# Performance work log

Measured on AMD Instinct MI355X. Metric: run time of the kernel, lower is better.

Reference implementation:

```python
import jax, jax.numpy as jnp
import numpy as np

KS = 2        # kernel_size
DIL = 1       # dilation
FILTERS = 512
Z_DIM = 128
B, C, T = 8, 512, 4096
TZ = T + 2 * (KS - 1)


def _conv1d(x, w, b):
    # x: (B, L, Cin), w: (ks, Cin, Cout) -> VALID conv, channels-last (keras Conv1D)
    y = jax.lax.conv_general_dilated(x, w, window_strides=(1,), padding='VALID',
                                     dimension_numbers=('NWC', 'WIO', 'NWC'))
    return y + b


def _adaptor(z, w1, b1, w2, b2):
    return _conv1d(jax.nn.relu(_conv1d(z, w1, b1)), w2, b2)


def setup_inputs() -> dict:
    key = jax.random.key(0)
    ks = jax.random.split(key, 10)
    lim = np.sqrt(6.0 / FILTERS)
    u = lambda k, shp: jax.random.uniform(k, shp, jnp.float32, -lim, lim)
    return {
        'x': jax.random.normal(ks[0], (B, C, T), jnp.float32),
        'z': jax.random.normal(ks[1], (B, TZ, Z_DIM), jnp.float32),
        'ww1': u(ks[2], (KS, Z_DIM, FILTERS)), 'wb1': jnp.zeros((FILTERS,), jnp.float32),
        'ww2': u(ks[3], (KS, FILTERS, FILTERS)), 'wb2': jnp.zeros((FILTERS,), jnp.float32),
        'bw1': u(ks[4], (KS, Z_DIM, FILTERS)), 'bb1': jnp.zeros((FILTERS,), jnp.float32),
        'bw2': u(ks[5], (KS, FILTERS, FILTERS)), 'bb2': jnp.zeros((FILTERS,), jnp.float32),
    }


def reference(x, z, ww1, wb1, ww2, wb2, bw1, bb1, bw2, bb2):
    m = x.shape[1]
    t = x.shape[2]
    pad = DIL * (KS - 1)
    xp = jnp.pad(x, ((0, 0), (0, 0), (0, pad)))
    end = t + pad
    # im2col-style unfold: (B, C*KS, T)
    xu = jnp.concatenate([xp[:, :, pad - i * DIL: end - i * DIL] for i in range(KS)], axis=1)
    weights = _adaptor(z, ww1, wb1, ww2, wb2)   # (B, T, F)
    bias = _adaptor(z, bw1, bb1, bw2, bb2)      # (B, T, F)
    y = jnp.matmul(xu, weights)                 # (B, C*KS, F)
    return y[:, :m, :] + bias[:, :m, :]
```

## Files before the change

kernel.cpp:

```cpp
#include <hip/hip_runtime.h>

typedef short short8 __attribute__((ext_vector_type(8)));
typedef float float4v __attribute__((ext_vector_type(4)));
typedef __attribute__((address_space(1))) const unsigned int gu32;
typedef __attribute__((address_space(3))) unsigned int lu32;

__device__ __forceinline__ unsigned short f2bf(float f) {
  unsigned int u = __builtin_bit_cast(unsigned int, f);
  u += 0x7FFFu + ((u >> 16) & 1u);
  return (unsigned short)(u >> 16);
}
__device__ __forceinline__ float bf2f(unsigned short s) {
  return __builtin_bit_cast(float, (unsigned int)s << 16);
}

__global__ __launch_bounds__(256) void prep_fused(
    const float* __restrict__ x,
    const float* __restrict__ z,
    const float* __restrict__ ww1, const float* __restrict__ ww2,
    const float* __restrict__ bw1, const float* __restrict__ bw2,
    unsigned short* __restrict__ xs, unsigned short* __restrict__ xz,
    float* __restrict__ rs,
    unsigned short* __restrict__ w1T, unsigned short* __restrict__ w2T,
    unsigned short* __restrict__ b1T, unsigned short* __restrict__ b2T,
    unsigned short* __restrict__ zb)
{
  if (blockIdx.x < 4096) {
    __shared__ float red[4];
    long long r = blockIdx.x;
    const float* xr = x + r * 4096;
    int t0 = threadIdx.x * 16;
    float v[17];
    const float4* xr4 = (const float4*)(xr + t0);
#pragma unroll
    for (int q = 0; q < 4; ++q) {
      float4 f = xr4[q];
      v[q * 4] = f.x; v[q * 4 + 1] = f.y; v[q * 4 + 2] = f.z; v[q * 4 + 3] = f.w;
    }
    v[16] = (t0 + 16 < 4096) ? xr[t0 + 16] : 0.f;
    unsigned int spk[8], zpk[8];
    float sum = 0.f;
#pragma unroll
    for (int q = 0; q < 8; ++q) {
      unsigned short s0 = f2bf(v[2 * q + 1]);
      unsigned short s1 = f2bf(v[2 * q + 2]);
      sum += bf2f(s0);
      sum += bf2f(s1);
      spk[q] = (unsigned int)s0 | ((unsigned int)s1 << 16);
      unsigned short z0 = (t0 == 0 && q == 0) ? (unsigned short)0 : f2bf(v[2 * q]);
      unsigned short z1 = f2bf(v[2 * q + 1]);
      zpk[q] = (unsigned int)z0 | ((unsigned int)z1 << 16);
    }
    *(uint4*)(xs + r * 4096 + t0)     = *(uint4*)(spk);
    *(uint4*)(xs + r * 4096 + t0 + 8) = *(uint4*)(spk + 4);
    *(uint4*)(xz + r * 4096 + t0)     = *(uint4*)(zpk);
    *(uint4*)(xz + r * 4096 + t0 + 8) = *(uint4*)(zpk + 4);
#pragma unroll
    for (int off = 32; off > 0; off >>= 1) sum += __shfl_down(sum, off);
    if ((threadIdx.x & 63) == 0) red[threadIdx.x >> 6] = sum;
    __syncthreads();
    if (threadIdx.x == 0) rs[r] = red[0] + red[1] + red[2] + red[3];
  } else {
    int i = (blockIdx.x - 4096) * 256 + threadIdx.x;
    if (i < 131072) {
      int n = i & 511, k = i >> 9;
      w1T[n * 256 + k] = f2bf(ww1[i]);
    } else if (i < 655360) {
      int j = i - 131072; int n = j & 511, k = j >> 9;
      w2T[n * 1024 + k] = f2bf(ww2[j]);
    } else if (i < 786432) {
      int j = i - 655360; int n = j & 511, k = j >> 9;
      b1T[n * 256 + k] = f2bf(bw1[j]);
    } else if (i < 1310720) {
      int j = i - 786432; int n = j & 511, k = j >> 9;
      b2T[n * 1024 + k] = f2bf(bw2[j]);
    } else {
      int j = i - 1310720;
      zb[j] = f2bf(z[j]);
    }
  }
}

template<int BM, int BN, bool RELU, bool OBF16, bool TRANS, bool SPLITK, int NH>
__global__ __launch_bounds__(256)
void gemm_bt(const unsigned short* __restrict__ A,
             const unsigned short* __restrict__ A2,
             const unsigned short* __restrict__ Bt,
             const float* __restrict__ biasv,
             void* __restrict__ outp,
             void* __restrict__ outp2,
             int M, int Kchunk, int RPB, int EXTRA, int BSCALE,
             int nHalf, int bRowMask,
             long long bStrideB, long long outBatchStride, int outLd)
{
  constexpr int WM = BM / 2, WN = BN / 2;
  constexpr int NI = WM / 16, NJ = WN / 16;
  constexpr int AI = BM / 64;
  constexpr int BI = BN / 64;
  constexpr int SA1 = BM * 32, SB1 = BN * 32;
  constexpr int STAGE = NH * (SA1 + SB1);
  constexpr int SMEMN = TRANS ? ((128 * 136 > STAGE) ? 128 * 136 : STAGE) : STAGE;
  __shared__ unsigned short smem[SMEMN];
  unsigned short* sB0 = smem + NH * SA1;

  const int tid  = threadIdx.x;
  const int lane = tid & 63;
  const int wave = tid >> 6;
  const int wm = wave >> 1, wn = wave & 1;
  const int lr = lane & 15, quad = lane >> 4;

  const int r0 = blockIdx.x * BM;
  const int n0 = blockIdx.y * BN;
  const int bb = r0 / RPB;
  const int Ktot = SPLITK ? Kchunk * gridDim.z : Kchunk;
  const int kOff = SPLITK ? blockIdx.z * Kchunk : 0;
  const long long bOffB = (long long)bb * bStrideB;
  const unsigned short* Ae = (nHalf && n0 >= nHalf) ? A2 : A;

  const int srow = lane >> 2;
  const int sg = (lane & 3) ^ (srow & 3);
  const unsigned short* gA[AI]; unsigned short* ldsA[AI];
#pragma unroll
  for (int c = 0; c < AI; ++c) {
    int instr = c * 4 + wave;
    int row = instr * 16 + srow;
    int r = r0 + row; if (r > M - 1) r = M - 1;
    gA[c] = Ae + ((long long)r + (long long)(r / RPB) * EXTRA) * BSCALE + kOff + sg * 8;
    ldsA[c] = smem + instr * 512;
  }
  const unsigned short* gB[BI]; unsigned short* ldsB[BI];
#pragma unroll
  for (int c = 0; c < BI; ++c) {
    int instr = c * 4 + wave;
    int row = instr * 16 + srow;
    gB[c] = Bt + (long long)((n0 + row) & bRowMask) * Ktot + bOffB + kOff + sg * 8;
    ldsB[c] = sB0 + instr * 512;
  }

  int aoff[NI], boff[NJ];
#pragma unroll
  for (int i = 0; i < NI; ++i) {
    int rr = wm * WM + i * 16 + lr;
    aoff[i] = rr * 32 + ((quad ^ (rr & 3)) * 8);
  }
#pragma unroll
  for (int j = 0; j < NJ; ++j) {
    int rr = wn * WN + j * 16 + lr;
    boff[j] = rr * 32 + ((quad ^ (rr & 3)) * 8);
  }

  float4v acc[NI][NJ];
  const float4v z4 = {0.f, 0.f, 0.f, 0.f};
#pragma unroll
  for (int i = 0; i < NI; ++i)
#pragma unroll
    for (int j = 0; j < NJ; ++j) acc[i][j] = z4;

  for (int k0 = 0; k0 < Kchunk; k0 += 32 * NH) {
#pragma unroll
    for (int h = 0; h < NH; ++h) {
#pragma unroll
      for (int c = 0; c < AI; ++c)
        __builtin_amdgcn_global_load_lds((gu32*)(gA[c] + k0 + h * 32),
                                         (lu32*)(ldsA[c] + h * SA1), 16, 0, 0);
#pragma unroll
      for (int c = 0; c < BI; ++c)
        __builtin_amdgcn_global_load_lds((gu32*)(gB[c] + k0 + h * 32),
                                         (lu32*)(ldsB[c] + h * SB1), 16, 0, 0);
    }
    __syncthreads();
#pragma unroll
    for (int h = 0; h < NH; ++h) {
      short8 af[NI], bfr[NJ];
#pragma unroll
      for (int i = 0; i < NI; ++i) af[i] = *(const short8*)(smem + h * SA1 + aoff[i]);
#pragma unroll
      for (int j = 0; j < NJ; ++j) bfr[j] = *(const short8*)(sB0 + h * SB1 + boff[j]);
#pragma unroll
      for (int i = 0; i < NI; ++i)
#pragma unroll
        for (int j = 0; j < NJ; ++j)
          acc[i][j] = __builtin_amdgcn_mfma_f32_16x16x32_bf16(af[i], bfr[j], acc[i][j], 0, 0, 0);
    }
    __syncthreads();
  }

  if (TRANS) {
    unsigned short* Ts = smem;
#pragma unroll
    for (int j = 0; j < NJ; ++j) {
      int fr = wn * WN + j * 16 + lr;
      float bv = biasv[n0 + fr];
#pragma unroll
      for (int i = 0; i < NI; ++i) {
        int tr = wm * WM + i * 16 + quad * 4;
        unsigned long long pk = 0;
#pragma unroll
        for (int g = 0; g < 4; ++g) {
          float vv = acc[i][j][g] + bv;
          if (RELU) vv = fmaxf(vv, 0.f);
          pk |= (unsigned long long)f2bf(vv) << (16 * g);
        }
        *(unsigned long long*)(Ts + fr * 136 + tr) = pk;
      }
    }
    __syncthreads();
    int fr = tid >> 1, sgg = tid & 1;
    int t0l = r0 - bb * RPB;
    unsigned short* dst = (unsigned short*)outp + (long long)bb * outBatchStride
                        + (long long)(n0 + fr) * outLd + t0l + sgg * 64;
    const unsigned short* srcp = Ts + fr * 136 + sgg * 64;
#pragma unroll
    for (int u = 0; u < 8; ++u)
      *(uint4*)(dst + u * 8) = *(const uint4*)(srcp + u * 8);
  } else {
    void* op = (SPLITK && blockIdx.z) ? outp2 : outp;
#pragma unroll
    for (int j = 0; j < NJ; ++j) {
      int n_g = n0 + wn * WN + j * 16 + lr;
      float bv = biasv ? biasv[n_g] : 0.f;
#pragma unroll
      for (int i = 0; i < NI; ++i) {
        int r_base = r0 + wm * WM + i * 16 + quad * 4;
#pragma unroll
        for (int g = 0; g < 4; ++g) {
          int r_g = r_base + g;
          if (r_g >= M) continue;
          float v = acc[i][j][g] + bv;
          if (RELU) v = fmaxf(v, 0.f);
          long long oidx = (long long)r_g * outLd + n_g;
          if (OBF16) ((unsigned short*)op)[oidx] = f2bf(v);
          else       ((float*)op)[oidx] = v;
        }
      }
    }
  }
}

__global__ __launch_bounds__(256) void final_gemm3(
    const unsigned short* __restrict__ p0,
    const unsigned short* __restrict__ p1,
    const unsigned short* __restrict__ h1b,
    const unsigned short* __restrict__ w2T,
    const unsigned short* __restrict__ b2T,
    const float* __restrict__ rs,
    const float* __restrict__ wb2,
    const float* __restrict__ bb2,
    float* __restrict__ out)
{
  constexpr int SA1 = 64 * 32, SB1 = 64 * 32;
  __shared__ unsigned short smem[4 * SA1 + 4 * SB1];
  const int tid = threadIdx.x;
  const int lane = tid & 63, wave = tid >> 6;
  const int wm = wave >> 1, wn = wave & 1;
  const int lr = lane & 15, quad = lane >> 4;
  const int r0 = blockIdx.x * 64, n0 = blockIdx.y * 64;

  const int srow = lane >> 2;
  const int sg = (lane & 3) ^ (srow & 3);
  const int row = wave * 16 + srow;
  const int rA = r0 + row;
  const int rB = n0 + row;
  const unsigned short* aP[3] = {
    p0 + (long long)rA * 1024 + sg * 8,
    p1 + (long long)rA * 1024 + sg * 8,
    h1b + ((long long)rA + (rA >> 9)) * 512 + sg * 8 };
  const unsigned short* bP[3] = {
    w2T + (long long)rB * 1024 + sg * 8,
    w2T + (long long)rB * 1024 + sg * 8,
    b2T + (long long)rB * 1024 + sg * 8 };
  unsigned short* ldsA = smem + wave * 512;
  unsigned short* ldsB = smem + 4 * SA1 + wave * 512;

  int aoff[2], boff[2];
#pragma unroll
  for (int i = 0; i < 2; ++i) {
    int rr = wm * 32 + i * 16 + lr;
    aoff[i] = rr * 32 + ((quad ^ (rr & 3)) * 8);
    int nn = wn * 32 + i * 16 + lr;
    boff[i] = 4 * SA1 + nn * 32 + ((quad ^ (nn & 3)) * 8);
  }

  float4v acc[2][2];
  const float4v z4 = {0.f, 0.f, 0.f, 0.f};
  acc[0][0] = z4; acc[0][1] = z4; acc[1][0] = z4; acc[1][1] = z4;

  for (int k0 = 0; k0 < 3072; k0 += 128) {
    int seg = k0 >> 10;
    int kk = k0 & 1023;
#pragma unroll
    for (int h = 0; h < 4; ++h) {
      __builtin_amdgcn_global_load_lds((gu32*)(aP[seg] + kk + h * 32),
                                       (lu32*)(ldsA + h * SA1), 16, 0, 0);
      __builtin_amdgcn_global_load_lds((gu32*)(bP[seg] + kk + h * 32),
                                       (lu32*)(ldsB + h * SB1), 16, 0, 0);
    }
    __syncthreads();
#pragma unroll
    for (int h = 0; h < 4; ++h) {
      short8 af[2], bfr[2];
      af[0] = *(const short8*)(smem + h * SA1 + aoff[0]);
      af[1] = *(const short8*)(smem + h * SA1 + aoff[1]);
      bfr[0] = *(const short8*)(smem + h * SB1 + boff[0]);
      bfr[1] = *(const short8*)(smem + h * SB1 + boff[1]);
#pragma unroll
      for (int i = 0; i < 2; ++i)
#pragma unroll
        for (int j = 0; j < 2; ++j)
          acc[i][j] = __builtin_amdgcn_mfma_f32_16x16x32_bf16(af[i], bfr[j], acc[i][j], 0, 0, 0);
    }
    __syncthreads();
  }

#pragma unroll
  for (int j = 0; j < 2; ++j) {
    int n_g = n0 + wn * 32 + j * 16 + lr;
    float w2b = wb2[n_g], bbv = bb2[n_g];
#pragma unroll
    for (int i = 0; i < 2; ++i) {
      int rb = r0 + wm * 32 + i * 16 + quad * 4;
#pragma unroll
      for (int g = 0; g < 4; ++g) {
        int r_g = rb + g;
        out[(long long)r_g * 512 + n_g] = acc[i][j][g] + rs[r_g] * w2b + bbv;
      }
    }
  }
}

extern "C" void kernel_launch(void* const* d_in, const int* in_sizes, int n_in,
                              void* d_out, int out_size, void* d_ws, size_t ws_size,
                              hipStream_t stream) {
  const float* x   = (const float*)d_in[0];
  const float* z   = (const float*)d_in[1];
  const float* ww1 = (const float*)d_in[2];
  const float* wb1 = (const float*)d_in[3];
  const float* ww2 = (const float*)d_in[4];
  const float* wb2 = (const float*)d_in[5];
  const float* bw1 = (const float*)d_in[6];
  const float* bb1 = (const float*)d_in[7];
  const float* bw2 = (const float*)d_in[8];
  const float* bb2 = (const float*)d_in[9];

  char* ws = (char*)d_ws;
  unsigned short* xs  = (unsigned short*)ws; ws += 16777216ll * 2;
  unsigned short* xz  = (unsigned short*)ws; ws += 16777216ll * 2;
  unsigned short* zb  = (unsigned short*)ws; ws += 4196352ll  * 2;
  unsigned short* h1T = (unsigned short*)ws; ws += 16777216ll * 2;
  unsigned short* h1b = (unsigned short*)ws; ws += 2101248ll  * 2;
  unsigned short* w2T = (unsigned short*)ws; ws += 524288ll * 2;
  unsigned short* b2T = (unsigned short*)ws; ws += 524288ll * 2;
  float* rs = (float*)ws;                    ws += 4096ll * 4;
  char* tail = ws;
  unsigned short* w1T = (unsigned short*)tail;
  unsigned short* b1T = (unsigned short*)tail + 131072;
  unsigned short* p0  = zb;
  unsigned short* p1  = (unsigned short*)tail;

  prep_fused<<<4096 + 21512, 256, 0, stream>>>(
      x, z, ww1, ww2, bw1, bw2, xs, xz, rs, w1T, w2T, b1T, b2T, zb);

  gemm_bt<128, 128, true, true, true, false, 2><<<dim3(256, 4), 256, 0, stream>>>(
      zb, nullptr, w1T, wb1, h1T, nullptr,
      32768, 256, 4096, 2, 128, 0, 0xFFFF, 0, 512ll * 4096, 4096);
  gemm_bt<64, 128, true, true, false, false, 2><<<dim3(65, 4), 256, 0, stream>>>(
      zb, nullptr, b1T, bb1, h1b, nullptr,
      4104, 256, 513, 3585, 128, 0, 0xFFFF, 0, 0, 512);
  gemm_bt<128, 128, false, true, false, true, 4><<<dim3(32, 8, 2), 256, 0, stream>>>(
      xs, xz, h1T, nullptr, p0, p1,
      4096, 2048, 512, 0, 4096, 512, 511, 512ll * 4096, 0, 1024);
  final_gemm3<<<dim3(64, 8), 256, 0, stream>>>(
      p0, p1, h1b, w2T, b2T, rs, wb2, bb2, (float*)d_out);
}
```

Before: 275.4 us.

## Merge x-conversion with first-layer GEMMs into one launch; row-pack split-K output

Splits the prep kernel so weight/z conversion runs first, then merges the x bf16 conversion/row-sum blocks with both first-layer adaptor GEMMs into a single heterogeneous 'mega' kernel. This cuts launches and lets the memory-bound x conversion overlap the compute-bound GEMMs. It also adds a ROWPACK epilogue for the split-K GEMM that stages bf16 results through LDS and writes 128-bit coalesced rows instead of scattered 2-byte stores. The mega kernel uses the largest shared-memory footprint for every block, which may reduce occupancy for the lightweight conversion blocks.

```diff
diff --git a/kernel.cpp b/kernel.cpp
--- a/kernel.cpp
+++ b/kernel.cpp
@@ -14,74 +14,209 @@
   return __builtin_bit_cast(float, (unsigned int)s << 16);
 }
 
-__global__ __launch_bounds__(256) void prep_fused(
-    const float* __restrict__ x,
-    const float* __restrict__ z,
+__global__ __launch_bounds__(256) void prep_w(
     const float* __restrict__ ww1, const float* __restrict__ ww2,
     const float* __restrict__ bw1, const float* __restrict__ bw2,
-    unsigned short* __restrict__ xs, unsigned short* __restrict__ xz,
-    float* __restrict__ rs,
+    const float* __restrict__ z,
     unsigned short* __restrict__ w1T, unsigned short* __restrict__ w2T,
     unsigned short* __restrict__ b1T, unsigned short* __restrict__ b2T,
     unsigned short* __restrict__ zb)
 {
-  if (blockIdx.x < 4096) {
-    __shared__ float red[4];
-    long long r = blockIdx.x;
-    const float* xr = x + r * 4096;
-    int t0 = threadIdx.x * 16;
-    float v[17];
-    const float4* xr4 = (const float4*)(xr + t0);
-#pragma unroll
-    for (int q = 0; q < 4; ++q) {
-      float4 f = xr4[q];
-      v[q * 4] = f.x; v[q * 4 + 1] = f.y; v[q * 4 + 2] = f.z; v[q * 4 + 3] = f.w;
-    }
-    v[16] = (t0 + 16 < 4096) ? xr[t0 + 16] : 0.f;
-    unsigned int spk[8], zpk[8];
-    float sum = 0.f;
-#pragma unroll
-    for (int q = 0; q < 8; ++q) {
-      unsigned short s0 = f2bf(v[2 * q + 1]);
-      unsigned short s1 = f2bf(v[2 * q + 2]);
-      sum += bf2f(s0);
-      sum += bf2f(s1);
-      spk[q] = (unsigned int)s0 | ((unsigned int)s1 << 16);
-      unsigned short z0 = (t0 == 0 && q == 0) ? (unsigned short)0 : f2bf(v[2 * q]);
-      unsigned short z1 = f2bf(v[2 * q + 1]);
-      zpk[q] = (unsigned int)z0 | ((unsigned int)z1 << 16);
-    }
-    *(uint4*)(xs + r * 4096 + t0)     = *(uint4*)(spk);
-    *(uint4*)(xs + r * 4096 + t0 + 8) = *(uint4*)(spk + 4);
-    *(uint4*)(xz + r * 4096 + t0)     = *(uint4*)(zpk);
-    *(uint4*)(xz + r * 4096 + t0 + 8) = *(uint4*)(zpk + 4);
-#pragma unroll
-    for (int off = 32; off > 0; off >>= 1) sum += __shfl_down(sum, off);
-    if ((threadIdx.x & 63) == 0) red[threadIdx.x >> 6] = sum;
-    __syncthreads();
-    if (threadIdx.x == 0) rs[r] = red[0] + red[1] + red[2] + red[3];
+  int i = blockIdx.x * 256 + threadIdx.x;
+  if (i < 131072) {
+    int n = i & 511, k = i >> 9;
+    w1T[n * 256 + k] = f2bf(ww1[i]);
+  } else if (i < 655360) {
+    int j = i - 131072; int n = j & 511, k = j >> 9;
+    w2T[n * 1024 + k] = f2bf(ww2[j]);
+  } else if (i < 786432) {
+    int j = i - 655360; int n = j & 511, k = j >> 9;
+    b1T[n * 256 + k] = f2bf(bw1[j]);
+  } else if (i < 1310720) {
+    int j = i - 786432; int n = j & 511, k = j >> 9;
+    b2T[n * 1024 + k] = f2bf(bw2[j]);
   } else {
-    int i = (blockIdx.x - 4096) * 256 + threadIdx.x;
-    if (i < 131072) {
-      int n = i & 511, k = i >> 9;
-      w1T[n * 256 + k] = f2bf(ww1[i]);
-    } else if (i < 655360) {
-      int j = i - 131072; int n = j & 511, k = j >> 9;
-      w2T[n * 1024 + k] = f2bf(ww2[j]);
-    } else if (i < 786432) {
-      int j = i - 655360; int n = j & 511, k = j >> 9;
-      b1T[n * 256 + k] = f2bf(bw1[j]);
-    } else if (i < 1310720) {
-      int j = i - 786432; int n = j & 511, k = j >> 9;
-      b2T[n * 1024 + k] = f2bf(bw2[j]);
-    } else {
-      int j = i - 1310720;
-      zb[j] = f2bf(z[j]);
-    }
-  }
-}
-
-template<int BM, int BN, bool RELU, bool OBF16, bool TRANS, bool SPLITK, int NH>
+    int j = i - 1310720;
+    zb[j] = f2bf(z[j]);
+  }
+}
+
+template<int BM, int BN, bool RELU, bool OBF16, bool TRANS, bool SPLITK, int NH, bool ROWPACK>
+__device__ __forceinline__ void gemm_core(
+    int bx, int by, int bz, int nzTot, unsigned short* smem,
+    const unsigned short* __restrict__ A,
+    const unsigned short* __restrict__ A2,
+    const unsigned short* __restrict__ Bt,
+    const float* __restrict__ biasv,
+    void* __restrict__ outp,
+    void* __restrict__ outp2,
+    int M, int Kchunk, int RPB, int EXTRA, int BSCALE,
+    int nHalf, int bRowMask,
+    long long bStrideB, long long outBatchStride, int outLd)
+{
+  constexpr int WM = BM / 2, WN = BN / 2;
+  constexpr int NI = WM / 16, NJ = WN / 16;
+  constexpr int AI = BM / 64;
+  constexpr int BI = BN / 64;
+  constexpr int SA1 = BM * 32, SB1 = BN * 32;
+  unsigned short* sB0 = smem + NH * SA1;
+
+  const int tid  = threadIdx.x;
+  const int lane = tid & 63;
+  const int wave = tid >> 6;
+  const int wm = wave >> 1, wn = wave & 1;
+  const int lr = lane & 15, quad = lane >> 4;
+
+  const int r0 = bx * BM;
+  const int n0 = by * BN;
+  const int bb = r0 / RPB;
+  const int Ktot = SPLITK ? Kchunk * nzTot : Kchunk;
+  const int kOff = SPLITK ? bz * Kchunk : 0;
+  const long long bOffB = (long long)bb * bStrideB;
+  const unsigned short* Ae = (nHalf && n0 >= nHalf) ? A2 : A;
+
+  const int srow = lane >> 2;
+  const int sg = (lane & 3) ^ (srow & 3);
+  const unsigned short* gA[AI]; unsigned short* ldsA[AI];
+#pragma unroll
+  for (int c = 0; c < AI; ++c) {
+    int instr = c * 4 + wave;
+    int row = instr * 16 + srow;
+    int r = r0 + row; if (r > M - 1) r = M - 1;
+    gA[c] = Ae + ((long long)r + (long long)(r / RPB) * EXTRA) * BSCALE + kOff + sg * 8;
+    ldsA[c] = smem + instr * 512;
+  }
+  const unsigned short* gB[BI]; unsigned short* ldsB[BI];
+#pragma unroll
+  for (int c = 0; c < BI; ++c) {
+    int instr = c * 4 + wave;
+    int row = instr * 16 + srow;
+    gB[c] = Bt + (long long)((n0 + row) & bRowMask) * Ktot + bOffB + kOff + sg * 8;
+    ldsB[c] = sB0 + instr * 512;
+  }
+
+  int aoff[NI], boff[NJ];
+#pragma unroll
+  for (int i = 0; i < NI; ++i) {
+    int rr = wm * WM + i * 16 + lr;
+    aoff[i] = rr * 32 + ((quad ^ (rr & 3)) * 8);
+  }
+#pragma unroll
+  for (int j = 0; j < NJ; ++j) {
+    int rr = wn * WN + j * 16 + lr;
+    boff[j] = rr * 32 + ((quad ^ (rr & 3)) * 8);
+  }
+
+  float4v acc[NI][NJ];
+  const float4v z4 = {0.f, 0.f, 0.f, 0.f};
+#pragma unroll
+  for (int i = 0; i < NI; ++i)
+#pragma unroll
+    for (int j = 0; j < NJ; ++j) acc[i][j] = z4;
+
+  for (int k0 = 0; k0 < Kchunk; k0 += 32 * NH) {
+#pragma unroll
+    for (int h = 0; h < NH; ++h) {
+#pragma unroll
+      for (int c = 0; c < AI; ++c)
+        __builtin_amdgcn_global_load_lds((gu32*)(gA[c] + k0 + h * 32),
+                                         (lu32*)(ldsA[c] + h * SA1), 16, 0, 0);
+#pragma unroll
+      for (int c = 0; c < BI; ++c)
+        __builtin_amdgcn_global_load_lds((gu32*)(gB[c] + k0 + h * 32),
+                                         (lu32*)(ldsB[c] + h * SB1), 16, 0, 0);
+    }
+    __syncthreads();
+#pragma unroll
+    for (int h = 0; h < NH; ++h) {
+      short8 af[NI], bfr[NJ];
+#pragma unroll
+      for (int i = 0; i < NI; ++i) af[i] = *(const short8*)(smem + h * SA1 + aoff[i]);
+#pragma unroll
+      for (int j = 0; j < NJ; ++j) bfr[j] = *(const short8*)(sB0 + h * SB1 + boff[j]);
+#pragma unroll
+      for (int i = 0; i < NI; ++i)
+#pragma unroll
+        for (int j = 0; j < NJ; ++j)
+          acc[i][j] = __builtin_amdgcn_mfma_f32_16x16x32_bf16(af[i], bfr[j], acc[i][j], 0, 0, 0);
+    }
+    __syncthreads();
+  }
+
+  if (TRANS) {
+    unsigned short* Ts = smem;
+#pragma unroll
+    for (int j = 0; j < NJ; ++j) {
+      int fr = wn * WN + j * 16 + lr;
+      float bv = biasv[n0 + fr];
+#pragma unroll
+      for (int i = 0; i < NI; ++i) {
+        int tr = wm * WM + i * 16 + quad * 4;
+        unsigned long long pk = 0;
+#pragma unroll
+        for (int g = 0; g < 4; ++g) {
+          float vv = acc[i][j][g] + bv;
+          if (RELU) vv = fmaxf(vv, 0.f);
+          pk |= (unsigned long long)f2bf(vv) << (16 * g);
+        }
+        *(unsigned long long*)(Ts + fr * 136 + tr) = pk;
+      }
+    }
+    __syncthreads();
+    int fr = tid >> 1, sgg = tid & 1;
+    int t0l = r0 - bb * RPB;
+    unsigned short* dst = (unsigned short*)outp + (long long)bb * outBatchStride
+                        + (long long)(n0 + fr) * outLd + t0l + sgg * 64;
+    const unsigned short* srcp = Ts + fr * 136 + sgg * 64;
+#pragma unroll
+    for (int u = 0; u < 8; ++u)
+      *(uint4*)(dst + u * 8) = *(const uint4*)(srcp + u * 8);
+  } else if (ROWPACK) {
+    void* op = (SPLITK && bz) ? outp2 : outp;
+    unsigned short* R = smem;
+#pragma unroll
+    for (int j = 0; j < NJ; ++j) {
+      int cc = wn * WN + j * 16 + lr;
+#pragma unroll
+      for (int i = 0; i < NI; ++i) {
+        int rrb = wm * WM + i * 16 + quad * 4;
+#pragma unroll
+        for (int g = 0; g < 4; ++g)
+          R[(rrb + g) * 136 + cc] = f2bf(acc[i][j][g]);
+      }
+    }
+    __syncthreads();
+    int rloc = tid >> 1, half = tid & 1;
+    unsigned short* dstp = (unsigned short*)op + (long long)(r0 + rloc) * outLd + n0 + half * 64;
+    const unsigned short* srcp = R + rloc * 136 + half * 64;
+#pragma unroll
+    for (int u = 0; u < 8; ++u)
+      *(uint4*)(dstp + u * 8) = *(const uint4*)(srcp + u * 8);
+  } else {
+    void* op = (SPLITK && bz) ? outp2 : outp;
+#pragma unroll
+    for (int j = 0; j < NJ; ++j) {
+      int n_g = n0 + wn * WN + j * 16 + lr;
+      float bv = biasv ? biasv[n_g] : 0.f;
+#pragma unroll
+      for (int i = 0; i < NI; ++i) {
+        int r_base = r0 + wm * WM + i * 16 + quad * 4;
+#pragma unroll
+        for (int g = 0; g < 4; ++g) {
+          int r_g = r_base + g;
+          if (r_g >= M) continue;
+          float v = acc[i][j][g] + bv;
+          if (RELU) v = fmaxf(v, 0.f);
+          long long oidx = (long long)r_g * outLd + n_g;
+          if (OBF16) ((unsigned short*)op)[oidx] = f2bf(v);
+          else       ((float*)op)[oidx] = v;
+        }
+      }
+    }
+  }
+}
+
+template<int BM, int BN, bool RELU, bool OBF16, bool TRANS, bool SPLITK, int NH, bool ROWPACK>
 __global__ __launch_bounds__(256)
 void gemm_bt(const unsigned short* __restrict__ A,
              const unsigned short* __restrict__ A2,
@@ -93,147 +228,78 @@
              int nHalf, int bRowMask,
              long long bStrideB, long long outBatchStride, int outLd)
 {
-  constexpr int WM = BM / 2, WN = BN / 2;
-  constexpr int NI = WM / 16, NJ = WN / 16;
-  constexpr int AI = BM / 64;
-  constexpr int BI = BN / 64;
-  constexpr int SA1 = BM * 32, SB1 = BN * 32;
-  constexpr int STAGE = NH * (SA1 + SB1);
-  constexpr int SMEMN = TRANS ? ((128 * 136 > STAGE) ? 128 * 136 : STAGE) : STAGE;
+  constexpr int STAGE = NH * (BM * 32 + BN * 32);
+  constexpr int REPK = (TRANS || ROWPACK) ? 128 * 136 : 0;
+  constexpr int SMEMN = (REPK > STAGE) ? REPK : STAGE;
   __shared__ unsigned short smem[SMEMN];
-  unsigned short* sB0 = smem + NH * SA1;
-
-  const int tid  = threadIdx.x;
-  const int lane = tid & 63;
-  const int wave = tid >> 6;
-  const int wm = wave >> 1, wn = wave & 1;
-  const int lr = lane & 15, quad = lane >> 4;
-
-  const int r0 = blockIdx.x * BM;
-  const int n0 = blockIdx.y * BN;
-  const int bb = r0 / RPB;
-  const int Ktot = SPLITK ? Kchunk * gridDim.z : Kchunk;
-  const int kOff = SPLITK ? blockIdx.z * Kchunk : 0;
-  const long long bOffB = (long long)bb * bStrideB;
-  const unsigned short* Ae = (nHalf && n0 >= nHalf) ? A2 : A;
-
-  const int srow = lane >> 2;
-  const int sg = (lane & 3) ^ (srow & 3);
-  const unsigned short* gA[AI]; unsigned short* ldsA[AI];
-#pragma unroll
-  for (int c = 0; c < AI; ++c) {
-    int instr = c * 4 + wave;
-    int row = instr * 16 + srow;
-    int r = r0 + row; if (r > M - 1) r = M - 1;
-    gA[c] = Ae + ((long long)r + (long long)(r / RPB) * EXTRA) * BSCALE + kOff + sg * 8;
-    ldsA[c] = smem + instr * 512;
-  }
-  const unsigned short* gB[BI]; unsigned short* ldsB[BI];
-#pragma unroll
-  for (int c = 0; c < BI; ++c) {
-    int instr = c * 4 + wave;
-    int row = instr * 16 + srow;
-    gB[c] = Bt + (long long)((n0 + row) & bRowMask) * Ktot + bOffB + kOff + sg * 8;
-    ldsB[c] = sB0 + instr * 512;
-  }
-
-  int aoff[NI], boff[NJ];
-#pragma unroll
-  for (int i = 0; i < NI; ++i) {
-    int rr = wm * WM + i * 16 + lr;
-    aoff[i] = rr * 32 + ((quad ^ (rr & 3)) * 8);
-  }
-#pragma unroll
-  for (int j = 0; j < NJ; ++j) {
-    int rr = wn * WN + j * 16 + lr;
-    boff[j] = rr * 32 + ((quad ^ (rr & 3)) * 8);
-  }
-
-  float4v acc[NI][NJ];
-  const float4v z4 = {0.f, 0.f, 0.f, 0.f};
-#pragma unroll
-  for (int i = 0; i < NI; ++i)
-#pragma unroll
-    for (int j = 0; j < NJ; ++j) acc[i][j] = z4;
-
-  for (int k0 = 0; k0 < Kchunk; k0 += 32 * NH) {
-#pragma unroll
-    for (int h = 0; h < NH; ++h) {
-#pragma unroll
-      for (int c = 0; c < AI; ++c)
-        __builtin_amdgcn_global_load_lds((gu32*)(gA[c] + k0 + h * 32),
-                                         (lu32*)(ldsA[c] + h * SA1), 16, 0, 0);
-#pragma unroll
-      for (int c = 0; c < BI; ++c)
-        __builtin_amdgcn_global_load_lds((gu32*)(gB[c] + k0 + h * 32),
-                                         (lu32*)(ldsB[c] + h * SB1), 16, 0, 0);
-    }
-    __syncthreads();
-#pragma unroll
-    for (int h = 0; h < NH; ++h) {
-      short8 af[NI], bfr[NJ];
-#pragma unroll
-      for (int i = 0; i < NI; ++i) af[i] = *(const short8*)(smem + h * SA1 + aoff[i]);
-#pragma unroll
-      for (int j = 0; j < NJ; ++j) bfr[j] = *(const short8*)(sB0 + h * SB1 + boff[j]);
-#pragma unroll
-      for (int i = 0; i < NI; ++i)
-#pragma unroll
-        for (int j = 0; j < NJ; ++j)
-          acc[i][j] = __builtin_amdgcn_mfma_f32_16x16x32_bf16(af[i], bfr[j], acc[i][j], 0, 0, 0);
-    }
-    __syncthreads();
-  }
-
-  if (TRANS) {
-    unsigned short* Ts = smem;
-#pragma unroll
-    for (int j = 0; j < NJ; ++j) {
-      int fr = wn * WN + j * 16 + lr;
-      float bv = biasv[n0 + fr];
-#pragma unroll
-      for (int i = 0; i < NI; ++i) {
-        int tr = wm * WM + i * 16 + quad * 4;
-        unsigned long long pk = 0;
-#pragma unroll
-        for (int g = 0; g < 4; ++g) {
-          float vv = acc[i][j][g] + bv;
-          if (RELU) vv = fmaxf(vv, 0.f);
-          pk |= (unsigned long long)f2bf(vv) << (16 * g);
-        }
-        *(unsigned long long*)(Ts + fr * 136 + tr) = pk;
-      }
-    }
-    __syncthreads();
-    int fr = tid >> 1, sgg = tid & 1;
-    int t0l = r0 - bb * RPB;
-    unsigned short* dst = (unsigned short*)outp + (long long)bb * outBatchStride
-                        + (long long)(n0 + fr) * outLd + t0l + sgg * 64;
-    const unsigned short* srcp = Ts + fr * 136 + sgg * 64;
-#pragma unroll
-    for (int u = 0; u < 8; ++u)
-      *(uint4*)(dst + u * 8) = *(const uint4*)(srcp + u * 8);
+  gemm_core<BM, BN, RELU, OBF16, TRANS, SPLITK, NH, ROWPACK>(
+      blockIdx.x, blockIdx.y, blockIdx.z, gridDim.z, smem,
+      A, A2, Bt, biasv, outp, outp2,
+      M, Kchunk, RPB, EXTRA, BSCALE, nHalf, bRowMask,
+      bStrideB, outBatchStride, outLd);
+}
+
+__global__ __launch_bounds__(256) void mega(
+    const float* __restrict__ x,
+    const unsigned short* __restrict__ zb,
+    const unsigned short* __restrict__ w1T,
+    const unsigned short* __restrict__ b1T,
+    const float* __restrict__ wb1,
+    const float* __restrict__ bb1,
+    unsigned short* __restrict__ h1T,
+    unsigned short* __restrict__ h1b,
+    unsigned short* __restrict__ xs,
+    unsigned short* __restrict__ xz,
+    float* __restrict__ rs)
+{
+  __shared__ unsigned short smem[17408];
+  int b = blockIdx.x;
+  if (b < 1024) {
+    gemm_core<128, 128, true, true, true, false, 2, false>(
+        b & 255, b >> 8, 0, 1, smem,
+        zb, nullptr, w1T, wb1, h1T, nullptr,
+        32768, 256, 4096, 2, 128, 0, 0xFFFF, 0, 512ll * 4096, 4096);
+  } else if (b < 1284) {
+    int idx = b - 1024;
+    gemm_core<64, 128, true, true, false, false, 2, false>(
+        idx % 65, idx / 65, 0, 1, smem,
+        zb, nullptr, b1T, bb1, h1b, nullptr,
+        4104, 256, 513, 3585, 128, 0, 0xFFFF, 0, 0, 512);
   } else {
-    void* op = (SPLITK && blockIdx.z) ? outp2 : outp;
-#pragma unroll
-    for (int j = 0; j < NJ; ++j) {
-      int n_g = n0 + wn * WN + j * 16 + lr;
-      float bv = biasv ? biasv[n_g] : 0.f;
-#pragma unroll
-      for (int i = 0; i < NI; ++i) {
-        int r_base = r0 + wm * WM + i * 16 + quad * 4;
-#pragma unroll
-        for (int g = 0; g < 4; ++g) {
-          int r_g = r_base + g;
-          if (r_g >= M) continue;
-          float v = acc[i][j][g] + bv;
-          if (RELU) v = fmaxf(v, 0.f);
-          long long oidx = (long long)r_g * outLd + n_g;
-          if (OBF16) ((unsigned short*)op)[oidx] = f2bf(v);
-          else       ((float*)op)[oidx] = v;
-        }
-      }
-    }
+    float* red = (float*)smem;
+    long long r = b - 1284;
+    const float* xr = x + r * 4096;
+    int t0 = threadIdx.x * 16;
+    float v[17];
+    const float4* xr4 = (const float4*)(xr + t0);
+#pragma unroll
+    for (int q = 0; q < 4; ++q) {
+      float4 f = xr4[q];
+      v[q * 4] = f.x; v[q * 4 + 1] = f.y; v[q * 4 + 2] = f.z; v[q * 4 + 3] = f.w;
+    }
+    v[16] = (t0 + 16 < 4096) ? xr[t0 + 16] : 0.f;
+    unsigned int spk[8], zpk[8];
+    float sum = 0.f;
+#pragma unroll
+    for (int q = 0; q < 8; ++q) {
+      unsigned short s0 = f2bf(v[2 * q + 1]);
+      unsigned short s1 = f2bf(v[2 * q + 2]);
+      sum += bf2f(s0);
+      sum += bf2f(s1);
+      spk[q] = (unsigned int)s0 | ((unsigned int)s1 << 16);
+      unsigned short z0 = (t0 == 0 && q == 0) ? (unsigned short)0 : f2bf(v[2 * q]);
+      unsigned short z1 = f2bf(v[2 * q + 1]);
+      zpk[q] = (unsigned int)z0 | ((unsigned int)z1 << 16);
+    }
+    *(uint4*)(xs + r * 4096 + t0)     = *(uint4*)(spk);
+    *(uint4*)(xs + r * 4096 + t0 + 8) = *(uint4*)(spk + 4);
+    *(uint4*)(xz + r * 4096 + t0)     = *(uint4*)(zpk);
+    *(uint4*)(xz + r * 4096 + t0 + 8) = *(uint4*)(zpk + 4);
+#pragma unroll
+    for (int off = 32; off > 0; off >>= 1) sum += __shfl_down(sum, off);
+    if ((threadIdx.x & 63) == 0) red[threadIdx.x >> 6] = sum;
+    __syncthreads();
+    if (threadIdx.x == 0) rs[r] = red[0] + red[1] + red[2] + red[3];
   }
 }
 
@@ -357,16 +423,9 @@
   unsigned short* p0  = zb;
   unsigned short* p1  = (unsigned short*)tail;
 
-  prep_fused<<<4096 + 21512, 256, 0, stream>>>(
-      x, z, ww1, ww2, bw1, bw2, xs, xz, rs, w1T, w2T, b1T, b2T, zb);
-
-  gemm_bt<128, 128, true, true, true, false, 2><<<dim3(256, 4), 256, 0, stream>>>(
-      zb, nullptr, w1T, wb1, h1T, nullptr,
-      32768, 256, 4096, 2, 128, 0, 0xFFFF, 0, 512ll * 4096, 4096);
-  gemm_bt<64, 128, true, true, false, false, 2><<<dim3(65, 4), 256, 0, stream>>>(
-      zb, nullptr, b1T, bb1, h1b, nullptr,
-      4104, 256, 513, 3585, 128, 0, 0xFFFF, 0, 0, 512);
-  gemm_bt<128, 128, false, true, false, true, 4><<<dim3(32, 8, 2), 256, 0, stream>>>(
+  prep_w<<<21512, 256, 0, stream>>>(ww1, ww2, bw1, bw2, z, w1T, w2T, b1T, b2T, zb);
+  mega<<<5380, 256, 0, stream>>>(x, zb, w1T, b1T, wb1, bb1, h1T, h1b, xs, xz, rs);
+  gemm_bt<128, 128, false, true, false, true, 4, true><<<dim3(32, 8, 2), 256, 0, stream>>>(
       xs, xz, h1T, nullptr, p0, p1,
       4096, 2048, 512, 0, 4096, 512, 511, 512ll * 4096, 0, 1024);
   final_gemm3<<<dim3(64, 8), 256, 0, stream>>>(
```

Result: faster. 252.2 us (-8.4%).
